# Optimization experiments

Hardware: AMD Instinct MI355X
Metric: run time of the kernel (lower is better)

Reference implementation:

```python
import jax, jax.numpy as jnp
import numpy as np

B, T, C = 2, 2048, 1024
H = 16
D = C // H  # head_dim = 64
SCALE = D ** -0.5


def setup_inputs() -> dict:
    key = jax.random.key(0)
    ks = jax.random.split(key, 5)
    s = 0.02
    return {
        "x": jax.random.normal(ks[0], (B, T, C), dtype=jnp.float32),
        "w_qkv": jax.random.normal(ks[1], (C, 3 * C), dtype=jnp.float32) * s,
        "b_qkv": jnp.zeros((3 * C,), dtype=jnp.float32),
        "w_proj": jax.random.normal(ks[2], (C, C), dtype=jnp.float32) * s,
        "b_proj": jnp.zeros((C,), dtype=jnp.float32),
    }


def reference(x, w_qkv, b_qkv, w_proj, b_proj):
    Bx, Tx, Cx = x.shape
    qkv = x @ w_qkv + b_qkv                      # [B,T,3C]
    q, k, v = jnp.split(qkv, 3, axis=-1)
    # [B,T,C] -> [B,H,T,D]
    q = q.reshape(Bx, Tx, H, D).transpose(0, 2, 1, 3)
    k = k.reshape(Bx, Tx, H, D).transpose(0, 2, 1, 3)
    v = v.reshape(Bx, Tx, H, D).transpose(0, 2, 1, 3)
    attn = jnp.einsum('bhqd,bhkd->bhqk', q, k) * SCALE
    causal = jnp.tril(jnp.ones((Tx, Tx), dtype=bool))
    attn = jnp.where(causal[None, None], attn, -jnp.inf)
    attn = jax.nn.softmax(attn, axis=-1)
    out = jnp.einsum('bhqk,bhkd->bhqd', attn, v)  # [B,H,T,D]
    out = out.transpose(0, 2, 1, 3).reshape(Bx, Tx, Cx)
    return out @ w_proj + b_proj
```

## Files before the change

### kernel.cpp

```cpp
#include <hip/hip_runtime.h>
#include <hip/hip_bf16.h>
#include <math.h>

#define T_SEQ 2048
#define NHEAD 16
#define HDIM  64
#define CDIM  1024
#define KDIM  1024
#define SCALE_L2E 0.1803368801111204f

typedef __attribute__((ext_vector_type(8))) short bf16x8;
typedef __attribute__((ext_vector_type(4))) float f32x4;
typedef __attribute__((ext_vector_type(16))) float f32x16;
typedef __attribute__((ext_vector_type(8))) unsigned short u16x8;
typedef __attribute__((ext_vector_type(4))) unsigned int u32x4;

__device__ __forceinline__ unsigned short f2bf(float f) {
    unsigned int u = __builtin_bit_cast(unsigned int, f);
    u += 0x7fffu + ((u >> 16) & 1u);
    return (unsigned short)(u >> 16);
}
__device__ __forceinline__ unsigned int cvt_pk_bf16(float lo, float hi_) {
    unsigned int r;
    asm("v_cvt_pk_bf16_f32 %0, %1, %2" : "=v"(r) : "v"(lo), "v"(hi_));
    return r;
}
__device__ __forceinline__ void pl32swap(unsigned int &a, unsigned int &b) {
    asm("v_permlane32_swap_b32 %0, %1" : "+v"(a), "+v"(b));
}
__device__ __forceinline__ void gld16(const unsigned short* g, unsigned short* l) {
    __builtin_amdgcn_global_load_lds(
        (const __attribute__((address_space(1))) unsigned int*)g,
        (__attribute__((address_space(3))) unsigned int*)l,
        16, 0, 0);
}

__global__ __launch_bounds__(256) void prep_x(const float* __restrict__ x,
                                              unsigned short* __restrict__ Xb) {
    size_t i = ((size_t)blockIdx.x * 256 + threadIdx.x) * 8;
    float4 a = *(const float4*)(x + i);
    float4 b = *(const float4*)(x + i + 4);
    u32x4 o;
    o[0] = cvt_pk_bf16(a.x, a.y);
    o[1] = cvt_pk_bf16(a.z, a.w);
    o[2] = cvt_pk_bf16(b.x, b.y);
    o[3] = cvt_pk_bf16(b.z, b.w);
    *(u32x4*)(Xb + i) = o;
}

template<int NC>
__global__ __launch_bounds__(256) void prep_w(const float* __restrict__ W,
                                              unsigned short* __restrict__ Wt) {
    __shared__ unsigned short Ls[64][72];
    const int n0 = blockIdx.x * 64, k0 = blockIdx.y * 64;
    const int t = threadIdx.x;
    {
        int kr = t >> 2, nc = (t & 3) * 16;
        #pragma unroll
        for (int j = 0; j < 4; j++) {
            float4 v = *(const float4*)(W + (size_t)(k0 + kr) * NC + n0 + nc + j * 4);
            Ls[nc + j*4 + 0][kr] = f2bf(v.x);
            Ls[nc + j*4 + 1][kr] = f2bf(v.y);
            Ls[nc + j*4 + 2][kr] = f2bf(v.z);
            Ls[nc + j*4 + 3][kr] = f2bf(v.w);
        }
    }
    __syncthreads();
    {
        int nr = t >> 2, kc = (t & 3) * 16;
        u16x8 o0 = *(const u16x8*)&Ls[nr][kc];
        u16x8 o1 = *(const u16x8*)&Ls[nr][kc + 8];
        *(u16x8*)(Wt + (size_t)(n0 + nr) * KDIM + k0 + kc)     = o0;
        *(u16x8*)(Wt + (size_t)(n0 + nr) * KDIM + k0 + kc + 8) = o1;
    }
}

template<int NC, int EPI>
__global__ __launch_bounds__(256) void gemm_k(
    const unsigned short* __restrict__ A, const unsigned short* __restrict__ Wt,
    const float* __restrict__ bias, float* __restrict__ Of,
    unsigned short* __restrict__ Qb, unsigned short* __restrict__ Kb,
    unsigned short* __restrict__ Vt)
{
    __shared__ unsigned short As[128 * 64];
    __shared__ unsigned short Bs[128 * 64];

    const int tid  = threadIdx.x;
    const int lane = tid & 63;
    const int wid  = tid >> 6;
    const int m0 = blockIdx.x * 128;
    const int n0 = blockIdx.y * 128;
    const int wm = (wid >> 1) * 64;
    const int wn = (wid & 1) * 64;
    const int rl = lane & 15;

    const int r8 = lane >> 3, s8 = lane & 7;
    const int swzs = (s8 ^ r8) * 8;

    f32x4 acc[4][4] = {};

    for (int k0 = 0; k0 < KDIM; k0 += 64) {
        #pragma unroll
        for (int c = 0; c < 4; c++) {
            int row = (wid << 5) + (c << 3) + r8;
            gld16(A  + (size_t)(m0 + row) * KDIM + k0 + swzs, &As[(size_t)((wid<<5)+(c<<3)) * 64]);
            gld16(Wt + (size_t)(n0 + row) * KDIM + k0 + swzs, &Bs[(size_t)((wid<<5)+(c<<3)) * 64]);
        }
        __syncthreads();
        #pragma unroll
        for (int kc = 0; kc < 2; kc++) {
            const int sb = kc * 4 + (lane >> 4);
            bf16x8 af[4], bfr[4];
            #pragma unroll
            for (int f = 0; f < 4; f++) {
                int sw = (sb ^ (rl & 7)) * 8;
                af[f]  = *(const bf16x8*)&As[(wm + f*16 + rl) * 64 + sw];
                bfr[f] = *(const bf16x8*)&Bs[(wn + f*16 + rl) * 64 + sw];
            }
            __builtin_amdgcn_s_setprio(1);
            #pragma unroll
            for (int i = 0; i < 4; i++)
                #pragma unroll
                for (int j = 0; j < 4; j++)
                    acc[i][j] = __builtin_amdgcn_mfma_f32_16x16x32_bf16(af[i], bfr[j], acc[i][j], 0, 0, 0);
            __builtin_amdgcn_s_setprio(0);
        }
        __syncthreads();
    }

    #pragma unroll
    for (int j = 0; j < 4; j++) {
        int gn = n0 + wn + j*16 + rl;
        float bv = bias[gn];
        #pragma unroll
        for (int i = 0; i < 4; i++) {
            int gm0 = m0 + wm + i*16 + (lane >> 4) * 4;
            #pragma unroll
            for (int r = 0; r < 4; r++) {
                float v = acc[i][j][r] + bv;
                int gm = gm0 + r;
                if (EPI == 0) {
                    int which = gn >> 10;
                    int cw = gn & 1023;
                    int h = cw >> 6, d = cw & 63;
                    int b = gm >> 11, t = gm & 2047;
                    size_t bh = (size_t)(b * NHEAD + h);
                    if (which == 0)      Qb[(bh * T_SEQ + t) * HDIM + d] = f2bf(v * SCALE_L2E);
                    else if (which == 1) Kb[(bh * T_SEQ + t) * HDIM + d] = f2bf(v);
                    else                 Vt[(bh * HDIM + d) * T_SEQ + t] = f2bf(v);
                } else {
                    Of[(size_t)gm * NC + gn] = v;
                }
            }
        }
    }
}

__global__ __launch_bounds__(128, 4) void attn_k(
    const unsigned short* __restrict__ Qb, const unsigned short* __restrict__ Kb,
    const unsigned short* __restrict__ Vt, unsigned short* __restrict__ AO)
{
    __shared__ unsigned short sbuf[2 * 4096];

    const int tid  = threadIdx.x;
    const int lane = tid & 63;
    const int w    = tid >> 6;
    const int bh   = blockIdx.x;
    const int qt   = 63 - blockIdx.y;
    const int ql   = lane & 31;
    const int hi   = lane >> 5;
    const int qg   = (qt << 5) + ql;

    const unsigned short* Qp = Qb + (size_t)bh * T_SEQ * HDIM;
    const unsigned short* Kp = Kb + (size_t)bh * T_SEQ * HDIM;
    const unsigned short* Vp = Vt + (size_t)bh * HDIM * T_SEQ;

    unsigned short* kbuf = sbuf + w * 4096;
    const char* kbB = (const char*)kbuf;
    const char* vbB = (const char*)(kbuf + 2048);

    const int r8 = lane >> 3, s8 = lane & 7;
    const int r4 = lane >> 2, s4 = lane & 3;
    const unsigned short* kSrc = Kp + (size_t)r8 * HDIM + ((s8 ^ r8) << 3);
    const unsigned short* vSrc = Vp + (size_t)r4 * T_SEQ + ((s4 ^ (r4 & 3)) << 3);

    auto issue_tile = [&](int t) {
        #pragma unroll
        for (int c = 0; c < 4; c++)
            gld16(kSrc + ((size_t)t << 11) + (c << 9), kbuf + (c << 9));
        #pragma unroll
        for (int c = 0; c < 4; c++)
            gld16(vSrc + ((size_t)c << 15) + (t << 5), kbuf + 2048 + (c << 9));
    };

    bf16x8 qf[4];
    #pragma unroll
    for (int dc = 0; dc < 4; dc++)
        qf[dc] = *(const bf16x8*)(Qp + (size_t)qg * HDIM + dc*16 + hi*8);

    float l_run = 0.f;
    f32x16 o0 = {}, o1 = {};

    if (w <= qt) {
        issue_tile(w);
        for (int t = w; t <= qt; t += 2) {
            asm volatile("s_waitcnt vmcnt(0)" ::: "memory");
            __builtin_amdgcn_sched_barrier(0);

            bf16x8 kf[4];
            #pragma unroll
            for (int dc = 0; dc < 4; dc++)
                kf[dc] = *(const bf16x8*)(kbB + ql*128 + (((dc << 1 | hi) ^ (ql & 7)) << 4));
            bf16x8 v00 = *(const bf16x8*)(vbB + ql*64        + (((0 | hi) ^ (ql & 3)) << 4));
            bf16x8 v01 = *(const bf16x8*)(vbB + ql*64        + (((2 | hi) ^ (ql & 3)) << 4));
            bf16x8 v10 = *(const bf16x8*)(vbB + (32+ql)*64   + (((0 | hi) ^ (ql & 3)) << 4));
            bf16x8 v11 = *(const bf16x8*)(vbB + (32+ql)*64   + (((2 | hi) ^ (ql & 3)) << 4));
            asm volatile("s_waitcnt lgkmcnt(0)" ::: "memory");
            __builtin_amdgcn_sched_barrier(0);

            if (t + 2 <= qt) issue_tile(t + 2);

            f32x16 s = {};
            __builtin_amdgcn_s_setprio(1);
            #pragma unroll
            for (int dc = 0; dc < 4; dc++)
                s = __builtin_amdgcn_mfma_f32_32x32x16_bf16(kf[dc], qf[dc], s, 0, 0, 0);
            __builtin_amdgcn_s_setprio(0);

            float p[16];
            if (t == qt) {
                #pragma unroll
                for (int r = 0; r < 16; r++) {
                    int kv = (t << 5) + (r & 3) + 8 * (r >> 2) + 4 * hi;
                    p[r] = (kv > qg) ? 0.f : exp2f(s[r]);
                }
            } else {
                #pragma unroll
                for (int r = 0; r < 16; r++) p[r] = exp2f(s[r]);
            }
            float r0 = (p[0]  + p[1])  + (p[2]  + p[3]);
            float r1 = (p[4]  + p[5])  + (p[6]  + p[7]);
            float r2 = (p[8]  + p[9])  + (p[10] + p[11]);
            float r3 = (p[12] + p[13]) + (p[14] + p[15]);
            l_run += (r0 + r1) + (r2 + r3);

            unsigned int c[8];
            #pragma unroll
            for (int i = 0; i < 8; i++) c[i] = cvt_pk_bf16(p[2*i], p[2*i+1]);
            pl32swap(c[0], c[2]);  pl32swap(c[1], c[3]);
            pl32swap(c[4], c[6]);  pl32swap(c[5], c[7]);
            u32x4 b0 = {c[0], c[1], c[2], c[3]};
            u32x4 b1 = {c[4], c[5], c[6], c[7]};
            bf16x8 pf0 = __builtin_bit_cast(bf16x8, b0);
            bf16x8 pf1 = __builtin_bit_cast(bf16x8, b1);

            __builtin_amdgcn_s_setprio(1);
            o0 = __builtin_amdgcn_mfma_f32_32x32x16_bf16(v00, pf0, o0, 0, 0, 0);
            o0 = __builtin_amdgcn_mfma_f32_32x32x16_bf16(v01, pf1, o0, 0, 0, 0);
            o1 = __builtin_amdgcn_mfma_f32_32x32x16_bf16(v10, pf0, o1, 0, 0, 0);
            o1 = __builtin_amdgcn_mfma_f32_32x32x16_bf16(v11, pf1, o1, 0, 0, 0);
            __builtin_amdgcn_s_setprio(0);
        }
    }

    __syncthreads();
    float* lf = (float*)sbuf;
    if (w == 1) {
        #pragma unroll
        for (int j = 0; j < 4; j++) {
            f32x4 a = { o0[4*j], o0[4*j+1], o0[4*j+2], o0[4*j+3] };
            *(f32x4*)(lf + (size_t)(j*64 + lane) * 4) = a;
        }
        #pragma unroll
        for (int j = 0; j < 4; j++) {
            f32x4 a = { o1[4*j], o1[4*j+1], o1[4*j+2], o1[4*j+3] };
            *(f32x4*)(lf + (size_t)((4+j)*64 + lane) * 4) = a;
        }
        lf[2048 + lane] = l_run;
    }
    __syncthreads();
    if (w == 0) {
        float l_all = l_run + lf[2048 + lane];
        l_all += __shfl_xor(l_all, 32);
        float linv = 1.f / l_all;
        const int b = bh >> 4, h = bh & 15;
        unsigned short* aop = AO + ((size_t)(b * T_SEQ + qg)) * CDIM + h * HDIM;
        #pragma unroll
        for (int qd = 0; qd < 4; qd++) {
            f32x4 x0 = *(const f32x4*)(lf + (size_t)(qd*64 + lane) * 4);
            f32x4 x1 = *(const f32x4*)(lf + (size_t)((4+qd)*64 + lane) * 4);
            uint2 w0, w1;
            w0.x = cvt_pk_bf16((o0[4*qd+0] + x0[0]) * linv, (o0[4*qd+1] + x0[1]) * linv);
            w0.y = cvt_pk_bf16((o0[4*qd+2] + x0[2]) * linv, (o0[4*qd+3] + x0[3]) * linv);
            w1.x = cvt_pk_bf16((o1[4*qd+0] + x1[0]) * linv, (o1[4*qd+1] + x1[1]) * linv);
            w1.y = cvt_pk_bf16((o1[4*qd+2] + x1[2]) * linv, (o1[4*qd+3] + x1[3]) * linv);
            *(uint2*)(aop + qd*8 + hi*4)      = w0;
            *(uint2*)(aop + 32 + qd*8 + hi*4) = w1;
        }
    }
}

extern "C" void kernel_launch(void* const* d_in, const int* in_sizes, int n_in,
                              void* d_out, int out_size, void* d_ws, size_t ws_size,
                              hipStream_t stream) {
    const float* x      = (const float*)d_in[0];
    const float* w_qkv  = (const float*)d_in[1];
    const float* b_qkv  = (const float*)d_in[2];
    const float* w_proj = (const float*)d_in[3];
    const float* b_proj = (const float*)d_in[4];
    float* out = (float*)d_out;

    const size_t MI = (size_t)1 << 20;
    unsigned short* base = (unsigned short*)d_ws;
    unsigned short* Qb  = base;
    unsigned short* Kb  = base + 4*MI;
    unsigned short* Vt  = base + 8*MI;
    unsigned short* Wqt = base + 12*MI;
    unsigned short* Wpt = base + 15*MI;
    unsigned short* Xb  = base + 16*MI;
    unsigned short* AO  = Xb;

    prep_x<<<dim3(2048), 256, 0, stream>>>(x, Xb);
    prep_w<3072><<<dim3(48, 16), 256, 0, stream>>>(w_qkv, Wqt);
    prep_w<1024><<<dim3(16, 16), 256, 0, stream>>>(w_proj, Wpt);
    gemm_k<3072, 0><<<dim3(32, 24), 256, 0, stream>>>(
        Xb, Wqt, b_qkv, nullptr, Qb, Kb, Vt);
    attn_k<<<dim3(32, 64), 128, 0, stream>>>(Qb, Kb, Vt, AO);
    gemm_k<1024, 1><<<dim3(32, 8), 256, 0, stream>>>(
        AO, Wpt, b_proj, out, nullptr, nullptr, nullptr);
}
```

Measured before the change: 113.7 us.

## Merge prep kernels into one launch and re-swizzle V tile LDS layout

Combines the three input-conversion kernels (x cast, two weight transposes) into a single launch that dispatches by block index, removing two kernel launches and the gaps between them. Separately, it changes how the V^T tile is loaded into LDS in the attention kernel: rows are laid out at 128-byte stride with an 8-way XOR swizzle matching the K tile, in place of the 64-byte rows with a 4-way swizzle. This is meant to reduce LDS bank conflicts on the V fragment reads and to make the global loads more coalesced. It risks mismatched fragment indexing if the new address mapping is wrong.

```diff
diff --git a/kernel.cpp b/kernel.cpp
--- a/kernel.cpp
+++ b/kernel.cpp
@@ -35,24 +35,33 @@
         16, 0, 0);
 }
 
-__global__ __launch_bounds__(256) void prep_x(const float* __restrict__ x,
-                                              unsigned short* __restrict__ Xb) {
-    size_t i = ((size_t)blockIdx.x * 256 + threadIdx.x) * 8;
-    float4 a = *(const float4*)(x + i);
-    float4 b = *(const float4*)(x + i + 4);
-    u32x4 o;
-    o[0] = cvt_pk_bf16(a.x, a.y);
-    o[1] = cvt_pk_bf16(a.z, a.w);
-    o[2] = cvt_pk_bf16(b.x, b.y);
-    o[3] = cvt_pk_bf16(b.z, b.w);
-    *(u32x4*)(Xb + i) = o;
-}
-
-template<int NC>
-__global__ __launch_bounds__(256) void prep_w(const float* __restrict__ W,
-                                              unsigned short* __restrict__ Wt) {
+__global__ __launch_bounds__(256) void prep_all(
+    const float* __restrict__ x,  unsigned short* __restrict__ Xb,
+    const float* __restrict__ wq, unsigned short* __restrict__ Wqt,
+    const float* __restrict__ wp, unsigned short* __restrict__ Wpt)
+{
     __shared__ unsigned short Ls[64][72];
-    const int n0 = blockIdx.x * 64, k0 = blockIdx.y * 64;
+    const int bid = blockIdx.x;
+    if (bid < 2048) {
+        size_t i = ((size_t)bid * 256 + threadIdx.x) * 8;
+        float4 a = *(const float4*)(x + i);
+        float4 b = *(const float4*)(x + i + 4);
+        u32x4 o;
+        o[0] = cvt_pk_bf16(a.x, a.y);
+        o[1] = cvt_pk_bf16(a.z, a.w);
+        o[2] = cvt_pk_bf16(b.x, b.y);
+        o[3] = cvt_pk_bf16(b.z, b.w);
+        *(u32x4*)(Xb + i) = o;
+        return;
+    }
+    const float* W; unsigned short* Wt; int NC, n0, k0;
+    if (bid < 2048 + 768) {
+        int b = bid - 2048;
+        W = wq; Wt = Wqt; NC = 3072; n0 = (b % 48) * 64; k0 = (b / 48) * 64;
+    } else {
+        int b = bid - 2816;
+        W = wp; Wt = Wpt; NC = 1024; n0 = (b % 16) * 64; k0 = (b / 16) * 64;
+    }
     const int t = threadIdx.x;
     {
         int kr = t >> 2, nc = (t & 3) * 16;
@@ -180,9 +189,9 @@
     const char* vbB = (const char*)(kbuf + 2048);
 
     const int r8 = lane >> 3, s8 = lane & 7;
-    const int r4 = lane >> 2, s4 = lane & 3;
-    const unsigned short* kSrc = Kp + (size_t)r8 * HDIM + ((s8 ^ r8) << 3);
-    const unsigned short* vSrc = Vp + (size_t)r4 * T_SEQ + ((s4 ^ (r4 & 3)) << 3);
+    const int key = s8 ^ r8;
+    const unsigned short* kSrc = Kp + (size_t)r8 * HDIM + (key << 3);
+    const unsigned short* vSrc = Vp + (size_t)((key >> 2) * 32 + r8) * T_SEQ + (key & 3) * 8;
 
     auto issue_tile = [&](int t) {
         #pragma unroll
@@ -190,7 +199,7 @@
             gld16(kSrc + ((size_t)t << 11) + (c << 9), kbuf + (c << 9));
         #pragma unroll
         for (int c = 0; c < 4; c++)
-            gld16(vSrc + ((size_t)c << 15) + (t << 5), kbuf + 2048 + (c << 9));
+            gld16(vSrc + ((size_t)c << 14) + (t << 5), kbuf + 2048 + (c << 9));
     };
 
     bf16x8 qf[4];
@@ -211,10 +220,10 @@
             #pragma unroll
             for (int dc = 0; dc < 4; dc++)
                 kf[dc] = *(const bf16x8*)(kbB + ql*128 + (((dc << 1 | hi) ^ (ql & 7)) << 4));
-            bf16x8 v00 = *(const bf16x8*)(vbB + ql*64        + (((0 | hi) ^ (ql & 3)) << 4));
-            bf16x8 v01 = *(const bf16x8*)(vbB + ql*64        + (((2 | hi) ^ (ql & 3)) << 4));
-            bf16x8 v10 = *(const bf16x8*)(vbB + (32+ql)*64   + (((0 | hi) ^ (ql & 3)) << 4));
-            bf16x8 v11 = *(const bf16x8*)(vbB + (32+ql)*64   + (((2 | hi) ^ (ql & 3)) << 4));
+            bf16x8 v00 = *(const bf16x8*)(vbB + ql*128 + (((0 + hi) ^ (ql & 7)) << 4));
+            bf16x8 v01 = *(const bf16x8*)(vbB + ql*128 + (((2 + hi) ^ (ql & 7)) << 4));
+            bf16x8 v10 = *(const bf16x8*)(vbB + ql*128 + (((4 + hi) ^ (ql & 7)) << 4));
+            bf16x8 v11 = *(const bf16x8*)(vbB + ql*128 + (((6 + hi) ^ (ql & 7)) << 4));
             asm volatile("s_waitcnt lgkmcnt(0)" ::: "memory");
             __builtin_amdgcn_sched_barrier(0);
 
@@ -320,9 +329,7 @@
     unsigned short* Xb  = base + 16*MI;
     unsigned short* AO  = Xb;
 
-    prep_x<<<dim3(2048), 256, 0, stream>>>(x, Xb);
-    prep_w<3072><<<dim3(48, 16), 256, 0, stream>>>(w_qkv, Wqt);
-    prep_w<1024><<<dim3(16, 16), 256, 0, stream>>>(w_proj, Wpt);
+    prep_all<<<dim3(3072), 256, 0, stream>>>(x, Xb, w_qkv, Wqt, w_proj, Wpt);
     gemm_k<3072, 0><<<dim3(32, 24), 256, 0, stream>>>(
         Xb, Wqt, b_qkv, nullptr, Qb, Kb, Vt);
     attn_k<<<dim3(32, 64), 128, 0, stream>>>(Qb, Kb, Vt, AO);
```

Result: faster. 110.5 us (-2.8%).
